# Kernel optimization log

Hardware: AMD Instinct MI355X
Metric: run time of the kernel (lower is better)

Reference implementation:

```python
import jax, jax.numpy as jnp
import numpy as np

N = 8192
F_IN = 512
F_OUT = 64
ALPHA = 0.2  # LeakyReLU negative slope
NEG_INF = -9e15


def setup_inputs() -> dict:
    key = jax.random.key(0)
    k1, k2, k3, k4 = jax.random.split(key, 4)
    inp = jax.random.normal(k1, (N, F_IN), dtype=jnp.float32)
    adj = jax.random.randint(k2, (N, N), 0, 2, dtype=jnp.int32)
    W = jax.random.normal(k3, (F_IN, F_OUT), dtype=jnp.float32) * 0.05
    a = jax.random.normal(k4, (2 * F_OUT, 1), dtype=jnp.float32) * 0.05
    return {"inp": inp, "adj": adj, "W": W, "a": a}


def reference(inp, adj, W, a):
    # h = W(inp): [N, F_OUT]
    h = inp @ W
    # a([h_i || h_j]) decomposes exactly into a1.h_i + a2.h_j, avoiding the
    # [N*N, 2F] concat tensor while computing identical math.
    f1 = h @ a[:F_OUT]        # [N, 1] source-node term
    f2 = h @ a[F_OUT:]        # [N, 1] target-node term
    e = jax.nn.leaky_relu(f1 + f2.T, negative_slope=ALPHA)  # [N, N]
    masked = jnp.where(adj > 0, e, jnp.float32(NEG_INF))
    attention = jax.nn.softmax(masked, axis=1)  # dropout is no-op at inference
    h_prime = attention @ h   # [N, F_OUT]
    return jax.nn.elu(h_prime)  # concat=True branch
```

## Files before the change

kernel.cpp:

```cpp
#include <hip/hip_runtime.h>

#define NN   8192
#define FIN  512
#define FOUT 64
#define KHALF 4096

typedef __attribute__((ext_vector_type(8)))  short short8;
typedef __attribute__((ext_vector_type(4)))  float floatx4;

__device__ __forceinline__ unsigned f2bf_u(float f) {
  union { float f; unsigned u; } v; v.f = f;
  return (v.u + 0x7fffu + ((v.u >> 16) & 1u)) >> 16;
}
__device__ __forceinline__ unsigned pack2(float a, float b) {
  return f2bf_u(a) | (f2bf_u(b) << 16);
}

__global__ __launch_bounds__(256) void k1_gemm_h(
    const float* __restrict__ inp, const float* __restrict__ W,
    const float* __restrict__ a,
    float* __restrict__ f1, float* __restrict__ f2,
    unsigned short* __restrict__ hT)
{
  __shared__ unsigned short at[32][72];
  __shared__ unsigned short wt[64][72];
  __shared__ float hsm[32][65];
  __shared__ float alds[2 * FOUT];

  const int tid   = threadIdx.x;
  const int rbase = blockIdx.x * 32;
  if (tid < 2 * FOUT) alds[tid] = a[tid];

  const int lane = tid & 63;
  const int wv   = tid >> 6;
  const int l15  = lane & 15;
  const int q    = lane >> 4;
  const int mi   = wv & 1;
  const int ni0  = (wv >> 1) * 2;

  const int r_a  = tid >> 3;
  const int k8   = (tid & 7) * 8;
  const int n_w  = tid & 63;
  const int kb_w = (tid >> 6) * 16;

  floatx4 acc0 = {0.f, 0.f, 0.f, 0.f};
  floatx4 acc1 = {0.f, 0.f, 0.f, 0.f};

  for (int kk0 = 0; kk0 < FIN; kk0 += 64) {
    __syncthreads();
    const float* ap = inp + (rbase + r_a) * FIN + kk0 + k8;
    float4 v0 = *(const float4*)ap;
    float4 v1 = *(const float4*)(ap + 4);
    *(uint4*)&at[r_a][k8] = make_uint4(pack2(v0.x, v0.y), pack2(v0.z, v0.w),
                                       pack2(v1.x, v1.y), pack2(v1.z, v1.w));
#pragma unroll
    for (int kk2 = 0; kk2 < 16; ++kk2)
      wt[n_w][kb_w + kk2] = (unsigned short)f2bf_u(W[(kk0 + kb_w + kk2) * FOUT + n_w]);
    __syncthreads();
#pragma unroll
    for (int ks = 0; ks < 2; ++ks) {
      short8 af = *(const short8*)&at[mi * 16 + l15][ks * 32 + q * 8];
      short8 b0 = *(const short8*)&wt[ni0 * 16 + l15][ks * 32 + q * 8];
      short8 b1 = *(const short8*)&wt[(ni0 + 1) * 16 + l15][ks * 32 + q * 8];
      acc0 = __builtin_amdgcn_mfma_f32_16x16x32_bf16(af, b0, acc0, 0, 0, 0);
      acc1 = __builtin_amdgcn_mfma_f32_16x16x32_bf16(af, b1, acc1, 0, 0, 0);
    }
  }

  {
    const int m0 = mi * 16 + q * 4;
    const int i0 = rbase + m0;
    {
      const int n = ni0 * 16 + l15;
#pragma unroll
      for (int rg = 0; rg < 4; ++rg) hsm[m0 + rg][n] = acc0[rg];
      *(uint2*)&hT[n * NN + i0] = make_uint2(pack2(acc0[0], acc0[1]),
                                             pack2(acc0[2], acc0[3]));
    }
    {
      const int n = (ni0 + 1) * 16 + l15;
#pragma unroll
      for (int rg = 0; rg < 4; ++rg) hsm[m0 + rg][n] = acc1[rg];
      *(uint2*)&hT[n * NN + i0] = make_uint2(pack2(acc1[0], acc1[1]),
                                             pack2(acc1[2], acc1[3]));
    }
  }
  __syncthreads();
  if (tid < 32) {
    float s1 = 0.f, s2 = 0.f;
#pragma unroll 8
    for (int c = 0; c < FOUT; ++c) {
      float hv = hsm[tid][c];
      s1 += hv * alds[c];
      s2 += hv * alds[FOUT + c];
    }
    f1[rbase + tid] = s1;
    f2[rbase + tid] = s2;
  }
}

__device__ __forceinline__ uint4 mkw8(const int4 A0, const int4 A1,
                                      const float4 F0, const float4 F1,
                                      const float f1v, float& lsum) {
  float e, w0, w1, w2, w3, w4, w5, w6, w7;
  e = f1v + F0.x; e = fmaxf(e, 0.2f * e); w0 = A0.x ? __expf(e) : 0.f;
  e = f1v + F0.y; e = fmaxf(e, 0.2f * e); w1 = A0.y ? __expf(e) : 0.f;
  e = f1v + F0.z; e = fmaxf(e, 0.2f * e); w2 = A0.z ? __expf(e) : 0.f;
  e = f1v + F0.w; e = fmaxf(e, 0.2f * e); w3 = A0.w ? __expf(e) : 0.f;
  e = f1v + F1.x; e = fmaxf(e, 0.2f * e); w4 = A1.x ? __expf(e) : 0.f;
  e = f1v + F1.y; e = fmaxf(e, 0.2f * e); w5 = A1.y ? __expf(e) : 0.f;
  e = f1v + F1.z; e = fmaxf(e, 0.2f * e); w6 = A1.z ? __expf(e) : 0.f;
  e = f1v + F1.w; e = fmaxf(e, 0.2f * e); w7 = A1.w ? __expf(e) : 0.f;
  lsum += ((w0 + w1) + (w2 + w3)) + ((w4 + w5) + (w6 + w7));
  return make_uint4(pack2(w0, w1), pack2(w2, w3), pack2(w4, w5), pack2(w6, w7));
}

__global__ __launch_bounds__(256, 4) void k2_attn(
    const int* __restrict__ adj,
    const float* __restrict__ f1g, const float* __restrict__ f2g,
    const unsigned short* __restrict__ hT,
    float* __restrict__ part, float* __restrict__ lpart)
{
  __shared__ __align__(16) unsigned char smem[33280];
  unsigned short (*wlds)[16][264] = (unsigned short (*)[16][264])smem;
  float* f2lds = (float*)(smem + 16896);
  __shared__ float lred[16][17];

  const int tid   = threadIdx.x;
  const int wv    = tid >> 6;
  const int lane  = tid & 63;
  const int l15   = lane & 15;
  const int q     = lane >> 4;
  const int rbase = (blockIdx.x >> 1) * 16;
  const int kh    = blockIdx.x & 1;
  const int kb    = kh * KHALF;

  const int r = tid >> 4;
  const int c = tid & 15;

  {
    const float4* src = (const float4*)(f2g + kb) + tid * 4;
    float4* dst = (float4*)f2lds + tid * 4;
    dst[0] = src[0]; dst[1] = src[1]; dst[2] = src[2]; dst[3] = src[3];
  }

  const int* ap  = adj + (size_t)(rbase + r) * NN + kb + c * 16;
  const float f1v = f1g[rbase + r];
  const unsigned short* hp = hT + (size_t)l15 * NN + kb + wv * 64 + q * 8;

  floatx4 acc[4];
#pragma unroll
  for (int ft = 0; ft < 4; ++ft) acc[ft] = (floatx4){0.f, 0.f, 0.f, 0.f};
  float lsum = 0.f;

  int4 A0 = *(const int4*)(ap);
  int4 A1 = *(const int4*)(ap + 4);
  int4 A2 = *(const int4*)(ap + 8);
  int4 A3 = *(const int4*)(ap + 12);

  __syncthreads();

  for (int it = 0; it < KHALF / 256; ++it) {
    const int nk = (it < KHALF / 256 - 1) ? (it + 1) * 256 : 0;
    int4 nA0 = *(const int4*)(ap + nk);
    int4 nA1 = *(const int4*)(ap + nk + 4);
    int4 nA2 = *(const int4*)(ap + nk + 8);
    int4 nA3 = *(const int4*)(ap + nk + 12);

    const float* fl = f2lds + it * 256 + c * 16;
    const int b = it & 1;
    {
      float4 F0 = *(const float4*)(fl);
      float4 F1 = *(const float4*)(fl + 4);
      *(uint4*)&wlds[b][r][c * 16] = mkw8(A0, A1, F0, F1, f1v, lsum);
    }
    {
      float4 F2 = *(const float4*)(fl + 8);
      float4 F3 = *(const float4*)(fl + 12);
      *(uint4*)&wlds[b][r][c * 16 + 8] = mkw8(A2, A3, F2, F3, f1v, lsum);
    }
    __syncthreads();

    const unsigned short* hit = hp + it * 256;
#pragma unroll
    for (int ks = 0; ks < 2; ++ks) {
      short8 af = *(const short8*)&wlds[b][l15][wv * 64 + ks * 32 + q * 8];
#pragma unroll
      for (int ft = 0; ft < 4; ++ft) {
        short8 bf = *(const short8*)(hit + ks * 32 + (size_t)ft * 16 * NN);
        acc[ft] = __builtin_amdgcn_mfma_f32_16x16x32_bf16(af, bf, acc[ft], 0, 0, 0);
      }
    }
    A0 = nA0; A1 = nA1; A2 = nA2; A3 = nA3;
  }

  __syncthreads();
  float (*pbuf)[1024] = (float (*)[1024])smem;

#pragma unroll
  for (int ft = 0; ft < 4; ++ft)
#pragma unroll
    for (int rg = 0; rg < 4; ++rg)
      pbuf[wv][(q * 4 + rg) * 64 + ft * 16 + l15] = acc[ft][rg];
  lred[r][c] = lsum;
  __syncthreads();

  {
    const int e0 = tid * 4;
    const int row = e0 >> 6;
    const int f0 = e0 & 63;
    float4 s0 = *(const float4*)&pbuf[0][e0];
    float4 s1 = *(const float4*)&pbuf[1][e0];
    float4 s2 = *(const float4*)&pbuf[2][e0];
    float4 s3 = *(const float4*)&pbuf[3][e0];
    s0.x += s1.x + s2.x + s3.x; s0.y += s1.y + s2.y + s3.y;
    s0.z += s1.z + s2.z + s3.z; s0.w += s1.w + s2.w + s3.w;
    *(float4*)(part + ((size_t)kh * NN + rbase + row) * 64 + f0) = s0;
  }
  if (tid < 16) {
    float s = 0.f;
#pragma unroll
    for (int i = 0; i < 16; ++i) s += lred[tid][i];
    lpart[(size_t)kh * NN + rbase + tid] = s;
  }
}

__global__ __launch_bounds__(256) void k3_combine(
    const float* __restrict__ part, const float* __restrict__ lpart,
    float* __restrict__ out)
{
  const int gid = blockIdx.x * 256 + threadIdx.x;
  const int i = gid >> 4;
  const int c = (gid & 15) * 4;
  const float inv = 1.f / (lpart[i] + lpart[NN + i]);
  float4 p0 = *(const float4*)(part + (size_t)i * 64 + c);
  float4 p1 = *(const float4*)(part + ((size_t)NN + i) * 64 + c);
  float4 v;
  v.x = (p0.x + p1.x) * inv; v.x = (v.x > 0.f) ? v.x : (__expf(v.x) - 1.f);
  v.y = (p0.y + p1.y) * inv; v.y = (v.y > 0.f) ? v.y : (__expf(v.y) - 1.f);
  v.z = (p0.z + p1.z) * inv; v.z = (v.z > 0.f) ? v.z : (__expf(v.z) - 1.f);
  v.w = (p0.w + p1.w) * inv; v.w = (v.w > 0.f) ? v.w : (__expf(v.w) - 1.f);
  *(float4*)(out + (size_t)i * 64 + c) = v;
}

extern "C" void kernel_launch(void* const* d_in, const int* in_sizes, int n_in,
                              void* d_out, int out_size, void* d_ws, size_t ws_size,
                              hipStream_t stream) {
  (void)in_sizes; (void)n_in; (void)out_size; (void)ws_size;
  const float* inp = (const float*)d_in[0];
  const int*   adj = (const int*)d_in[1];
  const float* W   = (const float*)d_in[2];
  const float* a   = (const float*)d_in[3];
  float* out = (float*)d_out;

  float* f1 = (float*)d_ws;
  float* f2 = f1 + NN;
  unsigned short* hT = (unsigned short*)(f2 + NN);
  float* part  = (float*)(hT + (size_t)FOUT * NN);
  float* lpart = part + 2 * (size_t)NN * FOUT;

  k1_gemm_h<<<NN / 32, 256, 0, stream>>>(inp, W, a, f1, f2, hT);
  k2_attn<<<(NN / 16) * 2, 256, 0, stream>>>(adj, f1, f2, hT, part, lpart);
  k3_combine<<<NN * FOUT / 4 / 256, 256, 0, stream>>>(part, lpart, out);
}
```

Before: 392.7 us.

## Drop K-split in attention kernel and fuse combine/ELU epilogue

New measurement: 392.3 us. About the same (-0.1%).

```diff
diff --git a/kernel.cpp b/kernel.cpp
--- a/kernel.cpp
+++ b/kernel.cpp
@@ -3,7 +3,6 @@
 #define NN   8192
 #define FIN  512
 #define FOUT 64
-#define KHALF 4096
 
 typedef __attribute__((ext_vector_type(8)))  short short8;
 typedef __attribute__((ext_vector_type(4)))  float floatx4;
@@ -115,38 +114,38 @@
   return make_uint4(pack2(w0, w1), pack2(w2, w3), pack2(w4, w5), pack2(w6, w7));
 }
 
-__global__ __launch_bounds__(256, 4) void k2_attn(
+__global__ __launch_bounds__(256, 2) void k2_attn(
     const int* __restrict__ adj,
     const float* __restrict__ f1g, const float* __restrict__ f2g,
     const unsigned short* __restrict__ hT,
-    float* __restrict__ part, float* __restrict__ lpart)
+    float* __restrict__ out)
 {
-  __shared__ __align__(16) unsigned char smem[33280];
+  __shared__ __align__(16) unsigned char smem[49664];
   unsigned short (*wlds)[16][264] = (unsigned short (*)[16][264])smem;
   float* f2lds = (float*)(smem + 16896);
   __shared__ float lred[16][17];
+  __shared__ float linv[16];
 
   const int tid   = threadIdx.x;
   const int wv    = tid >> 6;
   const int lane  = tid & 63;
   const int l15   = lane & 15;
   const int q     = lane >> 4;
-  const int rbase = (blockIdx.x >> 1) * 16;
-  const int kh    = blockIdx.x & 1;
-  const int kb    = kh * KHALF;
+  const int rbase = blockIdx.x * 16;
 
   const int r = tid >> 4;
   const int c = tid & 15;
 
   {
-    const float4* src = (const float4*)(f2g + kb) + tid * 4;
-    float4* dst = (float4*)f2lds + tid * 4;
-    dst[0] = src[0]; dst[1] = src[1]; dst[2] = src[2]; dst[3] = src[3];
-  }
-
-  const int* ap  = adj + (size_t)(rbase + r) * NN + kb + c * 16;
+    const float4* src = (const float4*)f2g;
+    float4* dst = (float4*)f2lds;
+#pragma unroll
+    for (int i = 0; i < 8; ++i) dst[tid + i * 256] = src[tid + i * 256];
+  }
+
+  const int* ap  = adj + (size_t)(rbase + r) * NN + c * 16;
   const float f1v = f1g[rbase + r];
-  const unsigned short* hp = hT + (size_t)l15 * NN + kb + wv * 64 + q * 8;
+  const unsigned short* hp = hT + (size_t)l15 * NN + wv * 64 + q * 8;
 
   floatx4 acc[4];
 #pragma unroll
@@ -160,8 +159,8 @@
 
   __syncthreads();
 
-  for (int it = 0; it < KHALF / 256; ++it) {
-    const int nk = (it < KHALF / 256 - 1) ? (it + 1) * 256 : 0;
+  for (int it = 0; it < NN / 256; ++it) {
+    const int nk = (it < NN / 256 - 1) ? (it + 1) * 256 : 0;
     int4 nA0 = *(const int4*)(ap + nk);
     int4 nA1 = *(const int4*)(ap + nk + 4);
     int4 nA2 = *(const int4*)(ap + nk + 8);
@@ -194,6 +193,7 @@
     A0 = nA0; A1 = nA1; A2 = nA2; A3 = nA3;
   }
 
+  lred[r][c] = lsum;
   __syncthreads();
   float (*pbuf)[1024] = (float (*)[1024])smem;
 
@@ -202,7 +202,12 @@
 #pragma unroll
     for (int rg = 0; rg < 4; ++rg)
       pbuf[wv][(q * 4 + rg) * 64 + ft * 16 + l15] = acc[ft][rg];
-  lred[r][c] = lsum;
+  if (tid < 16) {
+    float s = 0.f;
+#pragma unroll
+    for (int i = 0; i < 16; ++i) s += lred[tid][i];
+    linv[tid] = 1.f / s;
+  }
   __syncthreads();
 
   {
@@ -213,34 +218,18 @@
     float4 s1 = *(const float4*)&pbuf[1][e0];
     float4 s2 = *(const float4*)&pbuf[2][e0];
     float4 s3 = *(const float4*)&pbuf[3][e0];
-    s0.x += s1.x + s2.x + s3.x; s0.y += s1.y + s2.y + s3.y;
-    s0.z += s1.z + s2.z + s3.z; s0.w += s1.w + s2.w + s3.w;
-    *(float4*)(part + ((size_t)kh * NN + rbase + row) * 64 + f0) = s0;
-  }
-  if (tid < 16) {
-    float s = 0.f;
-#pragma unroll
-    for (int i = 0; i < 16; ++i) s += lred[tid][i];
-    lpart[(size_t)kh * NN + rbase + tid] = s;
-  }
-}
-
-__global__ __launch_bounds__(256) void k3_combine(
-    const float* __restrict__ part, const float* __restrict__ lpart,
-    float* __restrict__ out)
-{
-  const int gid = blockIdx.x * 256 + threadIdx.x;
-  const int i = gid >> 4;
-  const int c = (gid & 15) * 4;
-  const float inv = 1.f / (lpart[i] + lpart[NN + i]);
-  float4 p0 = *(const float4*)(part + (size_t)i * 64 + c);
-  float4 p1 = *(const float4*)(part + ((size_t)NN + i) * 64 + c);
-  float4 v;
-  v.x = (p0.x + p1.x) * inv; v.x = (v.x > 0.f) ? v.x : (__expf(v.x) - 1.f);
-  v.y = (p0.y + p1.y) * inv; v.y = (v.y > 0.f) ? v.y : (__expf(v.y) - 1.f);
-  v.z = (p0.z + p1.z) * inv; v.z = (v.z > 0.f) ? v.z : (__expf(v.z) - 1.f);
-  v.w = (p0.w + p1.w) * inv; v.w = (v.w > 0.f) ? v.w : (__expf(v.w) - 1.f);
-  *(float4*)(out + (size_t)i * 64 + c) = v;
+    const float inv = linv[row];
+    float4 v;
+    v.x = (s0.x + s1.x + s2.x + s3.x) * inv;
+    v.y = (s0.y + s1.y + s2.y + s3.y) * inv;
+    v.z = (s0.z + s1.z + s2.z + s3.z) * inv;
+    v.w = (s0.w + s1.w + s2.w + s3.w) * inv;
+    v.x = (v.x > 0.f) ? v.x : (__expf(v.x) - 1.f);
+    v.y = (v.y > 0.f) ? v.y : (__expf(v.y) - 1.f);
+    v.z = (v.z > 0.f) ? v.z : (__expf(v.z) - 1.f);
+    v.w = (v.w > 0.f) ? v.w : (__expf(v.w) - 1.f);
+    *(float4*)(out + (size_t)(rbase + row) * 64 + f0) = v;
+  }
 }
 
 extern "C" void kernel_launch(void* const* d_in, const int* in_sizes, int n_in,
@@ -256,10 +245,7 @@
   float* f1 = (float*)d_ws;
   float* f2 = f1 + NN;
   unsigned short* hT = (unsigned short*)(f2 + NN);
-  float* part  = (float*)(hT + (size_t)FOUT * NN);
-  float* lpart = part + 2 * (size_t)NN * FOUT;
 
   k1_gemm_h<<<NN / 32, 256, 0, stream>>>(inp, W, a, f1, f2, hT);
-  k2_attn<<<(NN / 16) * 2, 256, 0, stream>>>(adj, f1, f2, hT, part, lpart);
-  k3_combine<<<NN * FOUT / 4 / 256, 256, 0, stream>>>(part, lpart, out);
-}
+  k2_attn<<<NN / 16, 256, 0, stream>>>(adj, f1, f2, hT, out);
+}
```
